# Kernel tuning notes

Hardware: AMD Instinct MI355X
Metric: run time of the kernel (lower is better)

## Reference

```python
import jax, jax.numpy as jnp
import numpy as np
from jax import lax

B, CIN, HID, H, W, PS = 16, 64, 64, 128, 128, 8
PH, PW = H // PS, W // PS          # patch grid (16,16)
N = PH * PW                        # 256 patch tokens


def setup_inputs() -> dict:
    key = jax.random.key(0)
    ks = jax.random.split(key, 16)

    def wn(k, shape, s=0.02):
        return jax.random.normal(k, shape, jnp.float32) * s

    z = lambda n: jnp.zeros((n,), jnp.float32)
    return {
        "x": jax.random.normal(ks[0], (B, CIN, H, W), jnp.float32),
        "c": jax.random.normal(ks[1], (B, HID, H, W), jnp.float32),
        "h": jax.random.normal(ks[2], (B, HID, H, W), jnp.float32),
        "m": jax.random.normal(ks[3], (B, HID, H, W), jnp.float32),
        "conv_w": wn(ks[4], (4 * HID, CIN + HID, 3, 3)), "conv_b": z(4 * HID),
        "gn_w": jnp.ones((4 * HID,), jnp.float32), "gn_b": z(4 * HID),
        "qh_w": wn(ks[5], (HID, HID)), "qh_b": z(HID),
        "kh_w": wn(ks[6], (HID, HID)), "kh_b": z(HID),
        "vh_w": wn(ks[7], (HID, HID)), "vh_b": z(HID),
        "km_w": wn(ks[8], (HID, HID)), "km_b": z(HID),
        "vm_w": wn(ks[9], (HID, HID)), "vm_b": z(HID),
        "z_w": wn(ks[10], (2 * HID, 2 * HID)), "z_b": z(2 * HID),
        "m_w": wn(ks[11], (3 * HID, 3 * HID)), "m_b": z(3 * HID),
    }


def _conv1x1(t, w, b):
    return jnp.einsum('bchw,oc->bohw', t, w) + b[None, :, None, None]


def _pool(t):
    # Faithful to torch: view(B,C,N,-1).mean(-1) on row-major flattened HW
    b, c = t.shape[:2]
    return t.reshape(b, c, N, -1).mean(-1)  # (B,C,N)


def _cell(x, c, h, m, conv_w, conv_b, gn_w, gn_b,
          qh_w, qh_b, kh_w, kh_b, vh_w, vh_b, km_w, km_b, vm_w, vm_b,
          z_w, z_b, m_w, m_b):
    # --- ConvLSTM gating: 3x3 conv + GroupNorm(groups == channels) ---
    comb = jnp.concatenate([x, h], axis=1)
    cc = lax.conv_general_dilated(comb, conv_w, (1, 1), 'SAME',
                                  dimension_numbers=('NCHW', 'OIHW', 'NCHW'))
    cc = cc + conv_b[None, :, None, None]
    mu = cc.mean((2, 3), keepdims=True)
    var = cc.var((2, 3), keepdims=True)
    cc = (cc - mu) * lax.rsqrt(var + 1e-5)
    cc = cc * gn_w[None, :, None, None] + gn_b[None, :, None, None]
    i, f, g, o = jnp.split(cc, 4, axis=1)
    c_next = jax.nn.sigmoid(f) * c + jax.nn.sigmoid(i) * jnp.tanh(g)
    h_next = jax.nn.sigmoid(o) * jnp.tanh(c_next)

    # --- SA memory module ---
    Kp = _pool(_conv1x1(h_next, kh_w, kh_b))          # (B,C,N)
    Qp = _pool(_conv1x1(h_next, qh_w, qh_b))          # (B,C,N)
    Vp = _pool(_conv1x1(h_next, vh_w, vh_b))          # (B,C,N)
    Kmp = _pool(_conv1x1(m, km_w, km_b))
    Vmp = _pool(_conv1x1(m, vm_w, vm_b))

    A_h = jax.nn.softmax(jnp.einsum('bcn,bcm->bnm', Qp, Kp), axis=-1)   # (B,N,N)
    A_m = jax.nn.softmax(jnp.einsum('bcn,bcm->bnm', Qp, Kmp), axis=-1)
    Zh = jnp.einsum('bnm,bcm->bcn', A_h, Vp).reshape(-1, HID, PH, PW)
    Zm = jnp.einsum('bnm,bcm->bcn', A_m, Vmp).reshape(-1, HID, PH, PW)

    # bilinear upsample (half-pixel centers == torch align_corners=False)
    Zh = jax.image.resize(Zh, (Zh.shape[0], HID, H, W), 'bilinear')
    Zm = jax.image.resize(Zm, (Zm.shape[0], HID, H, W), 'bilinear')

    Z = _conv1x1(jnp.concatenate([Zh, Zm], axis=1), z_w, z_b)
    combined = _conv1x1(jnp.concatenate([Z, h_next], axis=1), m_w, m_b)
    mo, mg, mi = jnp.split(combined, 3, axis=1)
    mi = jax.nn.sigmoid(mi)
    new_m = (1 - mi) * m + mi * jnp.tanh(mg)
    new_h = jax.nn.sigmoid(mo) * new_m
    return new_h, c_next, new_m


def reference(x, c, h, m, conv_w, conv_b, gn_w, gn_b,
              qh_w, qh_b, kh_w, kh_b, vh_w, vh_b, km_w, km_b, vm_w, vm_b,
              z_w, z_b, m_w, m_b):
    return _cell(x, c, h, m, conv_w, conv_b, gn_w, gn_b,
                 qh_w, qh_b, kh_w, kh_b, vh_w, vh_b, km_w, km_b, vm_w, vm_b,
                 z_w, z_b, m_w, m_b)
```

## Files before the change

kernel.cpp:

```cpp
#include <hip/hip_runtime.h>
#include <hip/hip_bf16.h>
#include <math.h>

typedef __attribute__((ext_vector_type(4))) float f4;
typedef __attribute__((ext_vector_type(4))) float f32x4;
typedef __attribute__((ext_vector_type(8))) short bf16x8;

#define HSZ 128
#define WSZ 128
#define HW 16384

__device__ __forceinline__ float sigm(float x){ return 1.f/(1.f+__expf(-x)); }
__device__ __forceinline__ float tanh_fast(float x){ return 1.f - 2.f/(1.f+__expf(2.f*x)); }
__device__ __forceinline__ float bf_lo(unsigned u){ return __uint_as_float(u<<16); }
__device__ __forceinline__ float bf_hi(unsigned u){ return __uint_as_float(u & 0xffff0000u); }

__global__ void k_setup(const float* __restrict__ conv_w, const float* __restrict__ m_w,
                        __hip_bfloat16* __restrict__ wB, __hip_bfloat16* __restrict__ WhB){
  int idx = blockIdx.x*256 + threadIdx.x;
  if (idx < 294912){
    int kk = idx & 31;
    int oc = (idx>>5) & 255;
    int q  = idx >> 13;
    int dx = q % 3; int t2 = q / 3; int ck = t2 & 3; int dy = t2 >> 2;
    int ic = ck*32 + kk;
    wB[idx] = __float2bfloat16(conv_w[((oc*128+ic)*3+dy)*3+dx]);
  } else if (idx < 294912 + 12288){
    int j = idx - 294912;
    int o = j >> 6, ci = j & 63;
    WhB[j] = __float2bfloat16(m_w[o*192 + 128 + ci]);
  }
}

__global__ void k_w2(const float* __restrict__ m_w, const float* __restrict__ z_w,
                     const float* __restrict__ z_b, const float* __restrict__ m_b,
                     float* __restrict__ W2, float* __restrict__ bc){
  int idx = blockIdx.x*256 + threadIdx.x;
  if (idx < 24576){
    int o = idx >> 7, zi = idx & 127;
    float s = 0.f;
    for (int zo=0; zo<128; zo++) s += m_w[o*192+zo]*z_w[zo*128+zi];
    W2[idx] = s;
  } else if (idx < 24576 + 192){
    int o = idx - 24576;
    float s = m_b[o];
    for (int zo=0; zo<128; zo++) s += m_w[o*192+zo]*z_b[zo];
    bc[o] = s;
  }
}

__global__ __launch_bounds__(256) void k_im(const float* __restrict__ x,
    const float* __restrict__ h, __hip_bfloat16* __restrict__ im, int b0){
  __shared__ __hip_bfloat16 T[128*136];
  int bid = blockIdx.x; int y = bid & 127, bl = bid >> 7; int b = b0 + bl;
  int t = threadIdx.x;
  for (int idx=t; idx<4096; idx+=256){
    int c = idx>>5, xq = idx&31;
    const float* src = (c<64)? x : h; int cm = c&63;
    f4 v = *(const f4*)(src + ((((size_t)b*64+cm)*HSZ + y)*WSZ + xq*4));
    #pragma unroll
    for (int j=0;j<4;j++) T[(xq*4+j)*136 + c] = __float2bfloat16(v[j]);
  }
  __syncthreads();
  for (int idx=t; idx<2048; idx+=256){
    int xx = idx>>4, q = idx&15;
    uint4 v = *(const uint4*)&T[xx*136 + q*8];
    *(uint4*)(im + ((((size_t)bl*HSZ + y)*WSZ + xx)*128 + q*8)) = v;
  }
}

__global__ __launch_bounds__(256) void k_conv(const __hip_bfloat16* __restrict__ im,
    const __hip_bfloat16* __restrict__ wB, __hip_bfloat16* __restrict__ cc, int b0){
  __shared__ __align__(16) short LDS[17408];
  short* buf0 = LDS;
  short* buf1 = LDS + 5280;
  int bid = blockIdx.x;
  int y = bid & 127, bl = bid >> 7; int b = b0 + bl;
  int oc0 = blockIdx.y * 128;
  int t = threadIdx.x;
  int lane = t & 63, w = t >> 6;
  int ln15 = lane & 15, h8 = (lane>>4)*8;
  int ocw = (w>>1)*64, pxw = (w&1)*64;
  int px0 = t>>2, q0 = t&3;

  f32x4 acc[4][4];
  #pragma unroll
  for (int mi=0;mi<4;mi++)
    #pragma unroll
    for (int ni=0;ni<4;ni++) acc[mi][ni] = (f32x4){0.f,0.f,0.f,0.f};

  auto stage = [&](int s, short* dst){
    int dy = s>>2, ck = s&3;
    int yy = y + dy - 1;
    bool yok = (yy>=0) && (yy<HSZ);
    const __hip_bfloat16* rb = im + (((size_t)bl*HSZ + yy)*WSZ)*128 + ck*32;
    uint4 v0 = make_uint4(0u,0u,0u,0u);
    uint4 v1 = make_uint4(0u,0u,0u,0u);
    uint4 v2 = make_uint4(0u,0u,0u,0u);
    if (yok && px0>=1)       v0 = *(const uint4*)(rb + (size_t)(px0-1)*128 + q0*8);
    if (yok)                 v1 = *(const uint4*)(rb + (size_t)(px0+63)*128 + q0*8);
    if (yok && t<4)          v2 = *(const uint4*)(rb + (size_t)127*128 + q0*8);
    *(uint4*)&dst[px0*40 + q0*8]      = v0;
    *(uint4*)&dst[(px0+64)*40 + q0*8] = v1;
    if (t<16) *(uint4*)&dst[(128+(t>>2))*40 + q0*8] = v2;
  };
  auto compute = [&](int s, const short* src){
    #pragma unroll
    for (int dx=0; dx<3; dx++){
      const __hip_bfloat16* wp = wB + (((size_t)(s*3+dx)*256 + oc0 + ocw + ln15)*32 + h8);
      bf16x8 af[4], bfr[4];
      #pragma unroll
      for (int i=0;i<4;i++) af[i]  = *(const bf16x8*)(wp + (size_t)i*16*32);
      #pragma unroll
      for (int i=0;i<4;i++) bfr[i] = *(const bf16x8*)&src[(pxw + i*16 + ln15 + dx)*40 + h8];
      #pragma unroll
      for (int mi=0;mi<4;mi++)
        #pragma unroll
        for (int ni=0;ni<4;ni++)
          acc[mi][ni] = __builtin_amdgcn_mfma_f32_16x16x32_bf16(af[mi], bfr[ni], acc[mi][ni], 0, 0, 0);
    }
  };

  stage(0, buf0);
  __syncthreads();
  for (int s=0; s<12; s++){
    short* cur = (s&1)? buf1 : buf0;
    short* nxt = (s&1)? buf0 : buf1;
    if (s < 11) stage(s+1, nxt);
    compute(s, cur);
    __syncthreads();
  }

  __hip_bfloat16* OutL = (__hip_bfloat16*)LDS;
  int hv4 = (lane>>4)*4;
  #pragma unroll
  for (int mi=0;mi<4;mi++)
    #pragma unroll
    for (int ni=0;ni<4;ni++){
      #pragma unroll
      for (int r=0;r<4;r++)
        OutL[(ocw + mi*16 + hv4 + r)*136 + pxw + ni*16 + ln15] = __float2bfloat16(acc[mi][ni][r]);
    }
  __syncthreads();
  for (int idx=t; idx<2048; idx+=256){
    int oc = idx>>4, qc = idx&15;
    uint4 v = *(const uint4*)&OutL[oc*136 + qc*8];
    *(uint4*)(cc + ((((size_t)b*256 + oc0 + oc)*HSZ + y)*WSZ + qc*8)) = v;
  }
}

__global__ __launch_bounds__(256) void k_gnstats(const __hip_bfloat16* __restrict__ cc,
    const float* __restrict__ gn_w, const float* __restrict__ gn_b,
    float* __restrict__ scale, float* __restrict__ shift){
  int bc_ = blockIdx.x;
  const uint4* p = (const uint4*)(cc + (size_t)bc_*HW);
  float s=0.f, ss=0.f;
  for (int ch=threadIdx.x; ch<2048; ch+=256){
    uint4 u = p[ch];
    unsigned uw[4] = {u.x, u.y, u.z, u.w};
    #pragma unroll
    for (int w=0; w<4; w++){
      float a = bf_lo(uw[w]);
      float b2 = bf_hi(uw[w]);
      s += a + b2; ss += a*a + b2*b2;
    }
  }
  for (int off=1; off<64; off<<=1){ s += __shfl_xor(s, off); ss += __shfl_xor(ss, off); }
  __shared__ float rs_[4], rss_[4];
  int wv = threadIdx.x>>6, ln = threadIdx.x&63;
  if (ln==0){ rs_[wv]=s; rss_[wv]=ss; }
  __syncthreads();
  if (threadIdx.x==0){
    float S = rs_[0]+rs_[1]+rs_[2]+rs_[3];
    float SS = rss_[0]+rss_[1]+rss_[2]+rss_[3];
    float mu = S*(1.f/16384.f);
    float var = SS*(1.f/16384.f) - mu*mu;
    float r = rsqrtf(var + 1e-5f);
    int oc = bc_ & 255;
    float sc = gn_w[oc]*r;
    scale[bc_] = sc;
    shift[bc_] = gn_b[oc] - mu*sc;
  }
}

__global__ __launch_bounds__(256) void k_gate(const __hip_bfloat16* __restrict__ cc,
    const float* __restrict__ cin, const float* __restrict__ scale, const float* __restrict__ shift,
    float* __restrict__ out_c, float* __restrict__ out_h, float* __restrict__ poolh){
  int bid = blockIdx.x;
  int b = bid>>6, c = bid&63;
  size_t base_i = ((size_t)b*256 + c)*HW;
  const uint4* pi = (const uint4*)(cc + base_i);
  const uint4* pf = (const uint4*)(cc + base_i + (size_t)64*HW);
  const uint4* pg = (const uint4*)(cc + base_i + (size_t)128*HW);
  const uint4* po = (const uint4*)(cc + base_i + (size_t)192*HW);
  float ssi = scale[b*256+c],     shi = shift[b*256+c];
  float ssf = scale[b*256+64+c],  shf = shift[b*256+64+c];
  float ssg = scale[b*256+128+c], shg = shift[b*256+128+c];
  float sso = scale[b*256+192+c], sho = shift[b*256+192+c];
  size_t pbase = ((size_t)b*64 + c)*HW;
  const f4* pc_ = (const f4*)(cin + pbase);
  f4* oc_ = (f4*)(out_c + pbase);
  f4* oh_ = (f4*)(out_h + pbase);
  int lane = threadIdx.x & 63;
  for (int ch = threadIdx.x; ch < 2048; ch += 256){
    uint4 ui = pi[ch], uf = pf[ch], ug = pg[ch], uo = po[ch];
    unsigned iu[4]={ui.x,ui.y,ui.z,ui.w}, fu[4]={uf.x,uf.y,uf.z,uf.w};
    unsigned gu[4]={ug.x,ug.y,ug.z,ug.w}, ou[4]={uo.x,uo.y,uo.z,uo.w};
    f4 ca = pc_[ch*2], cb = pc_[ch*2+1];
    float cvv[8] = {ca[0],ca[1],ca[2],ca[3],cb[0],cb[1],cb[2],cb[3]};
    float rc[8], rh[8];
    #pragma unroll
    for (int w=0; w<4; w++){
      #pragma unroll
      for (int hl=0; hl<2; hl++){
        int k = w*2+hl;
        float iv = (hl? bf_hi(iu[w]) : bf_lo(iu[w]))*ssi + shi;
        float fv = (hl? bf_hi(fu[w]) : bf_lo(fu[w]))*ssf + shf;
        float gv = (hl? bf_hi(gu[w]) : bf_lo(gu[w]))*ssg + shg;
        float ov = (hl? bf_hi(ou[w]) : bf_lo(ou[w]))*sso + sho;
        float cn = sigm(fv)*cvv[k] + sigm(iv)*tanh_fast(gv);
        rc[k] = cn;
        rh[k] = sigm(ov)*tanh_fast(cn);
      }
    }
    f4 o0 = {rc[0],rc[1],rc[2],rc[3]}, o1 = {rc[4],rc[5],rc[6],rc[7]};
    f4 h0 = {rh[0],rh[1],rh[2],rh[3]}, h1 = {rh[4],rh[5],rh[6],rh[7]};
    oc_[ch*2] = o0; oc_[ch*2+1] = o1;
    oh_[ch*2] = h0; oh_[ch*2+1] = h1;
    float ps = ((rh[0]+rh[1])+(rh[2]+rh[3])) + ((rh[4]+rh[5])+(rh[6]+rh[7]));
    ps += __shfl_xor(ps, 1);
    ps += __shfl_xor(ps, 2);
    ps += __shfl_xor(ps, 4);
    if ((lane & 7) == 0) poolh[(size_t)bid*256 + (ch>>3)] = ps*(1.f/64.f);
  }
}

__global__ __launch_bounds__(256) void k_poolm(const float* __restrict__ m_in,
    float* __restrict__ poolm){
  int pc = blockIdx.x;
  const float* src = m_in + (size_t)pc*HW;
  float* dst = poolm + (size_t)pc*256;
  int n = threadIdx.x;
  const f4* p = (const f4*)(src + n*64);
  float s = 0.f;
  #pragma unroll
  for (int i=0;i<16;i++){ f4 v = p[i]; s += (v[0]+v[1]) + (v[2]+v[3]); }
  dst[n] = s*(1.f/64.f);
}

__global__ __launch_bounds__(256) void k_proj(const float* __restrict__ pool,
    const float* qw,const float* qb,const float* kw,const float* kb,
    const float* vw,const float* vb,const float* kmw,const float* kmb,
    const float* vmw,const float* vmb, float* __restrict__ proj){
  int bid = blockIdx.x;
  int p = bid % 5, b = bid / 5;
  const float* P = pool + (p>=3? 262144:0) + (size_t)b*16384;
  const float* W; const float* Bs;
  if (p==0){W=qw;Bs=qb;} else if(p==1){W=kw;Bs=kb;} else if(p==2){W=vw;Bs=vb;}
  else if (p==3){W=kmw;Bs=kmb;} else {W=vmw;Bs=vmb;}
  int n = threadIdx.x;
  float acc[64];
  #pragma unroll
  for (int o=0;o<64;o++) acc[o]=0.f;
  for (int c=0;c<64;c++){
    float pv = P[c*256+n];
    #pragma unroll
    for (int o=0;o<64;o++) acc[o] += W[o*64+c]*pv;
  }
  float* dst = proj + (size_t)p*262144 + (size_t)b*16384;
  #pragma unroll
  for (int o=0;o<64;o++) dst[o*256+n] = acc[o] + Bs[o];
}

__global__ __launch_bounds__(256) void k_scores(const float* __restrict__ proj, float* __restrict__ A){
  int n = blockIdx.x, ty = blockIdx.y, b = blockIdx.z;
  const float* Q = proj + (size_t)b*16384;
  const float* K = proj + (size_t)(ty==0?1:3)*262144 + (size_t)b*16384;
  int mm = threadIdx.x;
  float s = 0.f;
  for (int c=0;c<64;c++) s += Q[c*256+n]*K[c*256+mm];
  float mx = s;
  for (int off=1; off<64; off<<=1) mx = fmaxf(mx, __shfl_xor(mx, off));
  __shared__ float r1[4], r2[4];
  int wv = threadIdx.x>>6, ln = threadIdx.x&63;
  if (ln==0) r1[wv]=mx;
  __syncthreads();
  mx = fmaxf(fmaxf(r1[0],r1[1]),fmaxf(r1[2],r1[3]));
  float e = __expf(s-mx);
  float sm = e;
  for (int off=1; off<64; off<<=1) sm += __shfl_xor(sm, off);
  if (ln==0) r2[wv]=sm;
  __syncthreads();
  sm = r2[0]+r2[1]+r2[2]+r2[3];
  A[(((size_t)ty*16+b)*256+n)*256+mm] = e/sm;
}

__global__ __launch_bounds__(256) void k_apply(const float* __restrict__ proj,
    const float* __restrict__ A, float* __restrict__ Zcat){
  int ty = blockIdx.x, b = blockIdx.y, cq = blockIdx.z;
  const float* V = proj + (size_t)(ty==0?2:4)*262144 + (size_t)b*16384 + (size_t)cq*16*256;
  const float* Ar = A + (((size_t)ty*16+b)*256 + threadIdx.x)*256;
  float acc[16];
  #pragma unroll
  for (int c=0;c<16;c++) acc[c]=0.f;
  for (int mm=0; mm<256; mm++){
    float a = Ar[mm];
    #pragma unroll
    for (int c=0;c<16;c++) acc[c] += V[c*256+mm]*a;
  }
  float* dst = Zcat + ((size_t)b*128 + ty*64 + cq*16)*256 + threadIdx.x;
  #pragma unroll
  for (int c=0;c<16;c++) dst[c*256] = acc[c];
}

__global__ __launch_bounds__(256) void k_csmall(const float* __restrict__ Zcat,
    const float* __restrict__ W2, float* __restrict__ Cs){
  int oq = blockIdx.x, b = blockIdx.y;
  int o0 = oq*32;
  int n = threadIdx.x;
  float acc[32];
  #pragma unroll
  for (int o=0;o<32;o++) acc[o]=0.f;
  for (int zi=0; zi<128; zi++){
    float z = Zcat[((size_t)b*128+zi)*256 + n];
    #pragma unroll
    for (int o=0;o<32;o++) acc[o] += W2[(o0+o)*128 + zi]*z;
  }
  float* dst = Cs + ((size_t)b*192 + o0)*256 + n;
  #pragma unroll
  for (int o=0;o<32;o++) dst[o*256] = acc[o];
}

__global__ __launch_bounds__(256, 3) void k_final(
    const float* __restrict__ hn, const float* __restrict__ m_in,
    const __hip_bfloat16* __restrict__ WhB, const float* __restrict__ Cs,
    const float* __restrict__ bcv, float* __restrict__ out_h, float* __restrict__ out_m){
  __shared__ float rowF[64*69];
  __shared__ float CsL[192*36];
  int bid = blockIdx.x;
  int xh = bid & 1, y = (bid>>1) & 127, b = bid >> 8;
  int x0 = xh*64;
  int t = threadIdx.x, lane = t & 63, w = t >> 6;
  int ln15 = lane & 15, hi = lane >> 4, h8 = hi*8;

  float sy = (y+0.5f)*0.125f - 0.5f;
  int iy = (int)floorf(sy); float fy = sy - (float)iy;
  int ya = min(max(iy,0),15), yb = min(max(iy+1,0),15);

  for (int idx=t; idx<1024; idx+=256){
    int c = idx>>4, xq = idx&15;
    f4 v = *(const f4*)(hn + ((((size_t)b*64+c)*HSZ + y)*WSZ + x0 + xq*4));
    float* d = &rowF[c*69 + xq*4];
    d[0]=v[0]; d[1]=v[1]; d[2]=v[2]; d[3]=v[3];
  }
  for (int idx=t; idx<1536; idx+=256){
    int cp = idx>>3, rr = (idx>>2)&1, q = idx&3;
    int ry = rr? yb : ya;
    f4 v = *(const f4*)(Cs + (((size_t)b*192 + cp)*256 + ry*16 + q*4));
    *(f4*)&CsL[cp*36 + rr*16 + q*4] = v;
  }
  __syncthreads();

  bf16x8 bfr[2];
  #pragma unroll
  for (int ks=0; ks<2; ks++){
    union { bf16x8 v; __hip_bfloat16 e[8]; } u;
    #pragma unroll
    for (int j=0;j<8;j++)
      u.e[j] = __float2bfloat16(rowF[(ks*32 + h8 + j)*69 + w*16 + ln15]);
    bfr[ks] = u.v;
  }
  f32x4 acc[12];
  #pragma unroll
  for (int mt=0;mt<12;mt++) acc[mt] = (f32x4){0.f,0.f,0.f,0.f};
  #pragma unroll
  for (int ks=0; ks<2; ks++){
    #pragma unroll
    for (int mt=0; mt<12; mt++){
      bf16x8 af = *(const bf16x8*)(WhB + ((mt*16+ln15)*64 + ks*32 + h8));
      acc[mt] = __builtin_amdgcn_mfma_f32_16x16x32_bf16(af, bfr[ks], acc[mt], 0, 0, 0);
    }
  }

  int xg = x0 + w*16 + ln15;
  float sx = (xg+0.5f)*0.125f - 0.5f;
  int ix = (int)floorf(sx); float fx = sx - (float)ix;
  int xa = min(max(ix,0),15), xb2 = min(max(ix+1,0),15);
  float w00=(1.f-fy)*(1.f-fx), w01=(1.f-fy)*fx, w10=fy*(1.f-fx), w11=fy*fx;
  int o00 = xa, o01 = xb2, o10 = 16+xa, o11 = 16+xb2;
  #pragma unroll
  for (int mt=0; mt<4; mt++){
    #pragma unroll
    for (int r=0; r<4; r++){
      int c = mt*16 + hi*4 + r;
      const float* p0 = &CsL[c*36];
      const float* p1 = &CsL[(64+c)*36];
      const float* p2 = &CsL[(128+c)*36];
      float vo = acc[mt][r]   + p0[o00]*w00 + p0[o01]*w01 + p0[o10]*w10 + p0[o11]*w11 + bcv[c];
      float vg = acc[mt+4][r] + p1[o00]*w00 + p1[o01]*w01 + p1[o10]*w10 + p1[o11]*w11 + bcv[64+c];
      float vi = acc[mt+8][r] + p2[o00]*w00 + p2[o01]*w01 + p2[o10]*w10 + p2[o11]*w11 + bcv[128+c];
      size_t pix = (((size_t)b*64+c)*HSZ + y)*WSZ + xg;
      float mv = m_in[pix];
      float smi = sigm(vi);
      float nm = (1.f-smi)*mv + smi*tanh_fast(vg);
      float nh = sigm(vo)*nm;
      out_h[pix] = nh;
      out_m[pix] = nm;
    }
  }
}

extern "C" void kernel_launch(void* const* d_in, const int* in_sizes, int n_in,
                              void* d_out, int out_size, void* d_ws, size_t ws_size,
                              hipStream_t stream){
  (void)in_sizes; (void)n_in; (void)out_size;
  const float* x    = (const float*)d_in[0];
  const float* cst  = (const float*)d_in[1];
  const float* h    = (const float*)d_in[2];
  const float* m    = (const float*)d_in[3];
  const float* conv_w = (const float*)d_in[4];
  const float* gn_w = (const float*)d_in[6];
  const float* gn_b = (const float*)d_in[7];
  const float* qh_w = (const float*)d_in[8];  const float* qh_b = (const float*)d_in[9];
  const float* kh_w = (const float*)d_in[10]; const float* kh_b = (const float*)d_in[11];
  const float* vh_w = (const float*)d_in[12]; const float* vh_b = (const float*)d_in[13];
  const float* km_w = (const float*)d_in[14]; const float* km_b = (const float*)d_in[15];
  const float* vm_w = (const float*)d_in[16]; const float* vm_b = (const float*)d_in[17];
  const float* z_w  = (const float*)d_in[18]; const float* z_b  = (const float*)d_in[19];
  const float* m_w  = (const float*)d_in[20]; const float* m_b  = (const float*)d_in[21];

  float* out   = (float*)d_out;
  float* out_h = out;
  float* out_c = out + 16777216;
  float* out_m = out + 33554432;

  char* ws = (char*)d_ws;
  __hip_bfloat16* cc = (__hip_bfloat16*)ws;
  float* proj = (float*)(ws + 2097152);
  float* Amat = (float*)(ws + 7340032);
  float* Zcat = (float*)(ws + 15728640);
  float* Cs   = (float*)(ws + 17825792);
  float* pool = (float*)(ws + 134217728);

  bool big = (ws_size >= (size_t)202200000);
  size_t imOff = 134217728;
  size_t wOff  = big ? (imOff + 67108864) : 150994944;
  __hip_bfloat16* im  = (__hip_bfloat16*)(ws + imOff);
  __hip_bfloat16* wB  = (__hip_bfloat16*)(ws + wOff);
  __hip_bfloat16* WhB = (__hip_bfloat16*)(ws + wOff +  589824);
  float* W2   = (float*)(ws + wOff +  614400);
  float* bcv  = (float*)(ws + wOff +  712704);
  float* gnsc = (float*)(ws + wOff +  713472);
  float* gnsh = (float*)(ws + wOff +  729856);

  hipLaunchKernelGGL(k_setup, dim3(1200), dim3(256), 0, stream, conv_w, m_w, wB, WhB);
  hipLaunchKernelGGL(k_w2, dim3(97), dim3(256), 0, stream, m_w, z_w, z_b, m_b, W2, bcv);
  if (big){
    hipLaunchKernelGGL(k_im,   dim3(2048),    dim3(256), 0, stream, x, h, im, 0);
    hipLaunchKernelGGL(k_conv, dim3(2048, 2), dim3(256), 0, stream, im, wB, cc, 0);
  } else {
    for (int q = 0; q < 4; q++){
      hipLaunchKernelGGL(k_im,   dim3(512),    dim3(256), 0, stream, x, h, im, q*4);
      hipLaunchKernelGGL(k_conv, dim3(512, 2), dim3(256), 0, stream, im, wB, cc, q*4);
    }
  }
  hipLaunchKernelGGL(k_gnstats, dim3(4096), dim3(256), 0, stream, cc, gn_w, gn_b, gnsc, gnsh);
  hipLaunchKernelGGL(k_gate, dim3(1024), dim3(256), 0, stream, cc, cst, gnsc, gnsh, out_c, out_h, pool);
  hipLaunchKernelGGL(k_poolm, dim3(1024), dim3(256), 0, stream, m, pool + 262144);
  hipLaunchKernelGGL(k_proj, dim3(80), dim3(256), 0, stream, pool,
                     qh_w,qh_b,kh_w,kh_b,vh_w,vh_b,km_w,km_b,vm_w,vm_b, proj);
  hipLaunchKernelGGL(k_scores, dim3(256,2,16), dim3(256), 0, stream, proj, Amat);
  hipLaunchKernelGGL(k_apply, dim3(2,16,4), dim3(256), 0, stream, proj, Amat, Zcat);
  hipLaunchKernelGGL(k_csmall, dim3(6,16), dim3(256), 0, stream, Zcat, W2, Cs);
  hipLaunchKernelGGL(k_final, dim3(4096), dim3(256), 0, stream, out_h, m, WhB, Cs, bcv, out_h, out_m);
}
```

Baseline: 604.4 us.

## Compute two output rows per conv block to reuse weight fragments

Each conv block now computes two image rows instead of one. Each wave takes one row and all 128 pixels, so its accumulator tile grows from 4x4 to 4x8 MFMA tiles and each weight fragment loaded from global memory is reused across twice as many pixels. Two input rows are staged per step into a larger LDS double buffer, the grid is halved, and the epilogue writes the two rows out in turn. The cost is higher register pressure (128 accumulator floats per thread), more LDS use that may lower occupancy, and fewer blocks.

```diff
diff --git a/kernel.cpp b/kernel.cpp
--- a/kernel.cpp
+++ b/kernel.cpp
@@ -71,52 +71,64 @@
 
 __global__ __launch_bounds__(256) void k_conv(const __hip_bfloat16* __restrict__ im,
     const __hip_bfloat16* __restrict__ wB, __hip_bfloat16* __restrict__ cc, int b0){
-  __shared__ __align__(16) short LDS[17408];
+  __shared__ __align__(16) short LDS[21120];
   short* buf0 = LDS;
-  short* buf1 = LDS + 5280;
+  short* buf1 = LDS + 10560;
   int bid = blockIdx.x;
-  int y = bid & 127, bl = bid >> 7; int b = b0 + bl;
+  int y2 = bid & 63, bl = bid >> 6; int b = b0 + bl;
+  int y0 = y2*2;
   int oc0 = blockIdx.y * 128;
   int t = threadIdx.x;
   int lane = t & 63, w = t >> 6;
   int ln15 = lane & 15, h8 = (lane>>4)*8;
-  int ocw = (w>>1)*64, pxw = (w&1)*64;
-  int px0 = t>>2, q0 = t&3;
-
-  f32x4 acc[4][4];
+  int ocw = (w>>1)*64, row = w & 1;
+
+  f32x4 acc[4][8];
   #pragma unroll
   for (int mi=0;mi<4;mi++)
     #pragma unroll
-    for (int ni=0;ni<4;ni++) acc[mi][ni] = (f32x4){0.f,0.f,0.f,0.f};
+    for (int ni=0;ni<8;ni++) acc[mi][ni] = (f32x4){0.f,0.f,0.f,0.f};
 
   auto stage = [&](int s, short* dst){
     int dy = s>>2, ck = s&3;
-    int yy = y + dy - 1;
-    bool yok = (yy>=0) && (yy<HSZ);
-    const __hip_bfloat16* rb = im + (((size_t)bl*HSZ + yy)*WSZ)*128 + ck*32;
-    uint4 v0 = make_uint4(0u,0u,0u,0u);
-    uint4 v1 = make_uint4(0u,0u,0u,0u);
-    uint4 v2 = make_uint4(0u,0u,0u,0u);
-    if (yok && px0>=1)       v0 = *(const uint4*)(rb + (size_t)(px0-1)*128 + q0*8);
-    if (yok)                 v1 = *(const uint4*)(rb + (size_t)(px0+63)*128 + q0*8);
-    if (yok && t<4)          v2 = *(const uint4*)(rb + (size_t)127*128 + q0*8);
-    *(uint4*)&dst[px0*40 + q0*8]      = v0;
-    *(uint4*)&dst[(px0+64)*40 + q0*8] = v1;
-    if (t<16) *(uint4*)&dst[(128+(t>>2))*40 + q0*8] = v2;
+    int rbase = y0 + dy - 1;
+    const __hip_bfloat16* bp = im + ((size_t)bl*HSZ*WSZ)*128 + ck*32;
+    #pragma unroll
+    for (int k=0;k<4;k++){
+      int idx = t + k*256;
+      int s2 = (idx>=528)?1:0;
+      int id2 = idx - s2*528;
+      int px = id2>>2, q = id2&3;
+      int rr = rbase + s2;
+      uint4 v = make_uint4(0u,0u,0u,0u);
+      if (rr>=0 && rr<HSZ && px>=1 && px<129)
+        v = *(const uint4*)(bp + ((size_t)rr*WSZ + (px-1))*128 + q*8);
+      *(uint4*)&dst[s2*5280 + px*40 + q*8] = v;
+    }
+    if (t < 32){
+      int id2 = (1024+t) - 528;
+      int px = id2>>2, q = id2&3;
+      int rr = rbase + 1;
+      uint4 v = make_uint4(0u,0u,0u,0u);
+      if (rr>=0 && rr<HSZ && px>=1 && px<129)
+        v = *(const uint4*)(bp + ((size_t)rr*WSZ + (px-1))*128 + q*8);
+      *(uint4*)&dst[5280 + px*40 + q*8] = v;
+    }
   };
   auto compute = [&](int s, const short* src){
+    const short* sr = src + row*5280;
     #pragma unroll
     for (int dx=0; dx<3; dx++){
       const __hip_bfloat16* wp = wB + (((size_t)(s*3+dx)*256 + oc0 + ocw + ln15)*32 + h8);
-      bf16x8 af[4], bfr[4];
+      bf16x8 af[4], bfr[8];
       #pragma unroll
       for (int i=0;i<4;i++) af[i]  = *(const bf16x8*)(wp + (size_t)i*16*32);
       #pragma unroll
-      for (int i=0;i<4;i++) bfr[i] = *(const bf16x8*)&src[(pxw + i*16 + ln15 + dx)*40 + h8];
+      for (int n=0;n<8;n++) bfr[n] = *(const bf16x8*)&sr[(n*16 + ln15 + dx)*40 + h8];
       #pragma unroll
       for (int mi=0;mi<4;mi++)
         #pragma unroll
-        for (int ni=0;ni<4;ni++)
+        for (int ni=0;ni<8;ni++)
           acc[mi][ni] = __builtin_amdgcn_mfma_f32_16x16x32_bf16(af[mi], bfr[ni], acc[mi][ni], 0, 0, 0);
     }
   };
@@ -133,19 +145,24 @@
 
   __hip_bfloat16* OutL = (__hip_bfloat16*)LDS;
   int hv4 = (lane>>4)*4;
-  #pragma unroll
-  for (int mi=0;mi<4;mi++)
-    #pragma unroll
-    for (int ni=0;ni<4;ni++){
+  for (int p=0; p<2; p++){
+    if (row == p){
       #pragma unroll
-      for (int r=0;r<4;r++)
-        OutL[(ocw + mi*16 + hv4 + r)*136 + pxw + ni*16 + ln15] = __float2bfloat16(acc[mi][ni][r]);
-    }
-  __syncthreads();
-  for (int idx=t; idx<2048; idx+=256){
-    int oc = idx>>4, qc = idx&15;
-    uint4 v = *(const uint4*)&OutL[oc*136 + qc*8];
-    *(uint4*)(cc + ((((size_t)b*256 + oc0 + oc)*HSZ + y)*WSZ + qc*8)) = v;
+      for (int mi=0;mi<4;mi++)
+        #pragma unroll
+        for (int ni=0;ni<8;ni++){
+          #pragma unroll
+          for (int r=0;r<4;r++)
+            OutL[(ocw + mi*16 + hv4 + r)*136 + ni*16 + ln15] = __float2bfloat16(acc[mi][ni][r]);
+        }
+    }
+    __syncthreads();
+    for (int idx=t; idx<2048; idx+=256){
+      int oc = idx>>4, qc = idx&15;
+      uint4 v = *(const uint4*)&OutL[oc*136 + qc*8];
+      *(uint4*)(cc + ((((size_t)b*256 + oc0 + oc)*HSZ + (y0+p))*WSZ + qc*8)) = v;
+    }
+    __syncthreads();
   }
 }
 
@@ -457,11 +474,11 @@
   hipLaunchKernelGGL(k_w2, dim3(97), dim3(256), 0, stream, m_w, z_w, z_b, m_b, W2, bcv);
   if (big){
     hipLaunchKernelGGL(k_im,   dim3(2048),    dim3(256), 0, stream, x, h, im, 0);
-    hipLaunchKernelGGL(k_conv, dim3(2048, 2), dim3(256), 0, stream, im, wB, cc, 0);
+    hipLaunchKernelGGL(k_conv, dim3(1024, 2), dim3(256), 0, stream, im, wB, cc, 0);
   } else {
     for (int q = 0; q < 4; q++){
       hipLaunchKernelGGL(k_im,   dim3(512),    dim3(256), 0, stream, x, h, im, q*4);
-      hipLaunchKernelGGL(k_conv, dim3(512, 2), dim3(256), 0, stream, im, wB, cc, q*4);
+      hipLaunchKernelGGL(k_conv, dim3(256, 2), dim3(256), 0, stream, im, wB, cc, q*4);
     }
   }
   hipLaunchKernelGGL(k_gnstats, dim3(4096), dim3(256), 0, stream, cc, gn_w, gn_b, gnsc, gnsh);
```

Measured after the change: 708.5 us. 17.2% more time.
